# Performance work log

Hardware: AMD Instinct MI355X
Metric: run time of the kernel (lower is better)

The kernel has to match this reference:

```python
import jax, jax.numpy as jnp
import numpy as np

D_MODEL = 2048
NUM_HEADS = 16
HEAD_DIM = D_MODEL // NUM_HEADS  # 128
WINDOW = 1024
BATCH = 2
SEQ = 2048
NEG_INF = -1e9


def setup_inputs() -> dict:
    key = jax.random.key(0)
    ks = jax.random.split(key, 6)
    x = jax.random.normal(ks[0], (BATCH, SEQ, D_MODEL), dtype=jnp.float32)
    # RoPE frequencies (llama-style, theta=10000)
    inv_freq = 1.0 / (10000.0 ** (jnp.arange(0, HEAD_DIM, 2, dtype=jnp.float32) / HEAD_DIM))
    angles = jnp.arange(SEQ, dtype=jnp.float32)[:, None] * inv_freq[None, :]  # [S, hd/2]
    freqs_cos = jnp.cos(angles)
    freqs_sin = jnp.sin(angles)
    # additive causal mask [S, S]
    i = jnp.arange(SEQ)[:, None]
    j = jnp.arange(SEQ)[None, :]
    mask = jnp.where(j <= i, 0.0, NEG_INF).astype(jnp.float32)
    scale = 1.0 / np.sqrt(D_MODEL)
    w_q = jax.random.normal(ks[1], (D_MODEL, D_MODEL), dtype=jnp.float32) * scale
    w_k = jax.random.normal(ks[2], (D_MODEL, D_MODEL), dtype=jnp.float32) * scale
    w_v = jax.random.normal(ks[3], (D_MODEL, D_MODEL), dtype=jnp.float32) * scale
    w_o = jax.random.normal(ks[4], (D_MODEL, D_MODEL), dtype=jnp.float32) * scale
    return {"x": x, "freqs_cos": freqs_cos, "freqs_sin": freqs_sin, "mask": mask,
            "w_q": w_q, "w_k": w_k, "w_v": w_v, "w_o": w_o}


def _apply_rope(t, cos, sin):
    # t: [B, S, H, hd]; cos/sin: [S, hd/2]. Pairwise complex rotation.
    B, S, H, hd = t.shape
    tr = t.reshape(B, S, H, hd // 2, 2)
    a, b = tr[..., 0], tr[..., 1]
    c = cos[None, :, None, :]
    s = sin[None, :, None, :]
    out = jnp.stack([a * c - b * s, a * s + b * c], axis=-1)
    return out.reshape(B, S, H, hd)


def reference(x, freqs_cos, freqs_sin, mask, w_q, w_k, w_v, w_o):
    B, S, D = x.shape
    H, hd = NUM_HEADS, HEAD_DIM
    xq = (x @ w_q).reshape(B, S, H, hd)
    xk = (x @ w_k).reshape(B, S, H, hd)
    xv = (x @ w_v).reshape(B, S, H, hd)
    xq = _apply_rope(xq, freqs_cos, freqs_sin)
    xk = _apply_rope(xk, freqs_cos, freqs_sin)
    # scores: [B, H, S, S]
    scores = jnp.einsum("bqhd,bkhd->bhqk", xq, xk) / jnp.sqrt(jnp.asarray(hd, x.dtype))
    scores = scores + mask[None, None, :, :]
    # sliding-window mask: attend only to positions within WINDOW behind query
    i = jnp.arange(S)[:, None]
    j = jnp.arange(S)[None, :]
    sliding = (i - j >= 0) & (i - j < WINDOW)
    scores = jnp.where(sliding[None, None], scores, NEG_INF)
    probs = jax.nn.softmax(scores, axis=-1).astype(xq.dtype)
    out = jnp.einsum("bhqk,bkhd->bqhd", probs, xv).reshape(B, S, D)
    return out @ w_o
```

## Files before the change

kernel.cpp:

```cpp
#include <hip/hip_runtime.h>
#include <hip/hip_bf16.h>

typedef __attribute__((ext_vector_type(8))) short bf16x8;
typedef __attribute__((ext_vector_type(4))) float f32x4;
typedef unsigned short u16;
typedef unsigned int u32;

#define SEQ 2048
#define DMODEL 2048
#define NH 16
#define HD 128
#define NBATCH 2
#define WINDOW 1024

__device__ __forceinline__ float bf2f(u16 v) {
    union { u32 u; float f; } x; x.u = ((u32)v) << 16; return x.f;
}
__device__ __forceinline__ u16 f2bf(float f) {
    union { float f; u32 u; } x; x.f = f;
    u32 u = x.u;
    u32 r = (u + 0x7fffu + ((u >> 16) & 1u)) >> 16;
    return (u16)r;
}

__global__ __launch_bounds__(256) void cvt_f32_bf16(
    const float* __restrict__ in, u16* __restrict__ out)
{
    long i = ((long)blockIdx.x * 256 + threadIdx.x) * 8;
    float4 a = *(const float4*)(in + i);
    float4 b = *(const float4*)(in + i + 4);
    u16 v[8] = {f2bf(a.x), f2bf(a.y), f2bf(a.z), f2bf(a.w),
                f2bf(b.x), f2bf(b.y), f2bf(b.z), f2bf(b.w)};
    *(uint4*)(out + i) = *(uint4*)v;
}

__global__ __launch_bounds__(256) void transpose_f32_bf16(
    const float* __restrict__ in, u16* __restrict__ out, int R, int C)
{
    __shared__ u16 tile[64 * 72];
    const int c0 = blockIdx.x * 64, r0 = blockIdx.y * 64;
    const int t = threadIdx.x;
#pragma unroll
    for (int i = 0; i < 4; ++i) {
        int ch = i * 256 + t;
        int r = ch >> 4, c4 = (ch & 15) * 4;
        float4 v = *(const float4*)(in + (long)(r0 + r) * C + c0 + c4);
        tile[r * 72 + c4 + 0] = f2bf(v.x);
        tile[r * 72 + c4 + 1] = f2bf(v.y);
        tile[r * 72 + c4 + 2] = f2bf(v.z);
        tile[r * 72 + c4 + 3] = f2bf(v.w);
    }
    __syncthreads();
#pragma unroll
    for (int i = 0; i < 4; ++i) {
        int ch = i * 256 + t;
        int oc = ch >> 4, sg = (ch & 15) * 4;
        u16 vals[4];
#pragma unroll
        for (int j = 0; j < 4; ++j) vals[j] = tile[(sg + j) * 72 + oc];
        *(uint2*)(out + (long)(c0 + oc) * R + r0 + sg) = *(uint2*)vals;
    }
}

#define GLD16(gp, lp) __builtin_amdgcn_global_load_lds( \
    (const __attribute__((address_space(1))) u32*)(gp), \
    (__attribute__((address_space(3))) u32*)(lp), 16, 0, 0)
#define BAR() __builtin_amdgcn_s_barrier()
#define WAITV(n) asm volatile("s_waitcnt vmcnt(" #n ")" ::: "memory")

template <int MODE>
__global__ __launch_bounds__(512, 2) void gemm256(
    const u16* __restrict__ A, const u16* __restrict__ Bt,
    u16* __restrict__ OutB, float* __restrict__ OutF,
    const float* __restrict__ cosb, const float* __restrict__ sinb)
{
    extern __shared__ u16 sm[];
    const int t = threadIdx.x;
    const int w = t >> 6, l = t & 63;
    const int g = l >> 4, l15 = l & 15;
    const int wr = w >> 1, wc = w & 1;

    const int NWG = (MODE == 1) ? 768 : 256;
    const int cpx = NWG / 8;
    int bid = blockIdx.x;
    int wg = (bid & 7) * cpx + (bid >> 3);
    int z, m_t, n_t;
    if (MODE == 1) { z = wg >> 8; int rem = wg & 255; n_t = rem >> 4; m_t = rem & 15; }
    else           { z = 0; n_t = wg >> 4; m_t = wg & 15; }
    const int m0 = m_t * 256, n0 = n_t * 128;
    const u16* Ab = A + (long)m0 * 2048;
    const u16* Bb = Bt + (long)z * (2048L * 2048) + (long)n0 * 2048;

    const int r0 = t >> 3;
    const int kk16 = (t & 7) ^ (r0 & 7);
    const long g_off = (long)r0 * 2048 + kk16 * 8;
    const int lds_l = w * 512;
    const int sw = (l15 & 7) << 3;

#define STAGE(bufS_, ktS_) do { \
    const u16* _ga = Ab + (long)(ktS_) * 64 + g_off; \
    u16* _la = sm + (bufS_) * 24576 + lds_l; \
    GLD16(_ga,              _la); \
    GLD16(_ga +  64 * 2048, _la + 4096); \
    GLD16(_ga + 128 * 2048, _la + 8192); \
    GLD16(_ga + 192 * 2048, _la + 12288); \
    const u16* _gb = Bb + (long)(ktS_) * 64 + g_off; \
    u16* _lb = sm + (bufS_) * 24576 + 16384 + lds_l; \
    GLD16(_gb,              _lb); \
    GLD16(_gb + 64 * 2048,  _lb + 4096); \
} while (0)

    bf16x8 af[4][2], bfr[2][2];
    f32x4 acc[4][4] = {};

#define LDA_ALL(bufv) { const u16* _ba = sm + (bufv) * 24576; \
    _Pragma("unroll") for (int i = 0; i < 4; ++i) { \
        int row = wr * 64 + i * 16 + l15; \
        _Pragma("unroll") for (int kx = 0; kx < 2; ++kx) \
            af[i][kx] = *(const bf16x8*)(_ba + row * 64 + ((kx * 32 + g * 8) ^ sw)); } }

#define LDB_H(q, bufv) { const u16* _bb = sm + (bufv) * 24576 + 16384; \
    _Pragma("unroll") for (int j = 0; j < 2; ++j) { \
        int row = wc * 64 + (q) * 32 + j * 16 + l15; \
        _Pragma("unroll") for (int kx = 0; kx < 2; ++kx) \
            bfr[j][kx] = *(const bf16x8*)(_bb + row * 64 + ((kx * 32 + g * 8) ^ sw)); } }

#define MM(q) { __builtin_amdgcn_s_setprio(1); \
    _Pragma("unroll") for (int i = 0; i < 4; ++i) \
    _Pragma("unroll") for (int j = 0; j < 2; ++j) \
    _Pragma("unroll") for (int kx = 0; kx < 2; ++kx) \
        acc[i][(q) * 2 + j] = __builtin_amdgcn_mfma_f32_16x16x32_bf16( \
            af[i][kx], bfr[j][kx], acc[i][(q) * 2 + j], 0, 0, 0); \
    __builtin_amdgcn_s_setprio(0); }

    STAGE(0, 0); STAGE(1, 1);
    WAITV(6); BAR();

    int buf = 0, bufS = 2;
#pragma unroll 1
    for (int kt = 0; kt < 32; ++kt) {
        const int ktS = (kt + 2 <= 31) ? (kt + 2) : 31;
        LDA_ALL(buf); LDB_H(0, buf);
        STAGE(bufS, ktS);
        BAR(); MM(0); BAR();
        LDB_H(1, buf);
        WAITV(6);
        BAR(); MM(1); BAR();
        buf  = (buf  == 2) ? 0 : buf + 1;
        bufS = (bufS == 2) ? 0 : bufS + 1;
    }

#pragma unroll
    for (int mt = 0; mt < 4; ++mt) {
#pragma unroll
        for (int nt = 0; nt < 4; ++nt) {
#pragma unroll
            for (int r = 0; r < 4; ++r) {
                int m = m0 + wr * 64 + mt * 16 + g * 4 + r;
                int n = n0 + wc * 64 + nt * 16 + l15;
                float v = acc[mt][nt][r];
                if (MODE == 0) {
                    OutF[(long)m * 2048 + n] = v;
                } else {
                    int b = m >> 11, s = m & 2047;
                    int h = n >> 7,  d = n & 127;
                    float pv = __shfl_xor(v, 1);
                    if (z < 2) {
                        int p = d >> 1;
                        float cc = cosb[s * 64 + p];
                        float ss = sinb[s * 64 + p];
                        v = ((d & 1) == 0) ? (v * cc - pv * ss) : (pv * ss + v * cc);
                    }
                    long zoff = (long)z * (NBATCH * NH * SEQ * HD);
                    if (z == 2)
                        OutB[zoff + ((long)(b * NH + h) * HD + d) * SEQ + s] = f2bf(v);
                    else
                        OutB[zoff + ((long)(b * NH + h) * SEQ + s) * HD + d] = f2bf(v);
                }
            }
        }
    }
#undef STAGE
#undef LDA_ALL
#undef LDB_H
#undef MM
}

__global__ __launch_bounds__(256, 2) void attn_kernel(
    const u16* __restrict__ Q,
    const u16* __restrict__ K,
    const u16* __restrict__ Vt,
    u16* __restrict__ Out)
{
    __shared__ u16 k_lds[64 * 136];
    __shared__ u16 vt_lds[128 * 72];
    __shared__ u16 p_lds[4 * 16 * 72];
    const int t = threadIdx.x, w = t >> 6, l = t & 63;
    const int g = l >> 4, l15 = l & 15;
    const int q0 = blockIdx.x * 64;
    const int bh = blockIdx.y;
    const int qbase = q0 + w * 16;
    const u16* Qb = Q + (long)bh * SEQ * HD;
    const u16* Kb = K + (long)bh * SEQ * HD;
    const u16* Vb = Vt + (long)bh * HD * SEQ;
    u16* pw = p_lds + w * 16 * 72;

    bf16x8 qf[4];
#pragma unroll
    for (int kk = 0; kk < 4; ++kk)
        qf[kk] = *(const bf16x8*)(Qb + (long)(qbase + l15) * HD + kk * 32 + g * 8);

    f32x4 of[8] = {};
    float mrow[4] = {-1e30f, -1e30f, -1e30f, -1e30f};
    float lrow[4] = {0.f, 0.f, 0.f, 0.f};
    const float scale = 0.088388347648318447f;

    const int t0 = (q0 >= WINDOW) ? ((q0 - (WINDOW - 1)) >> 6) : 0;
    const int t1 = q0 >> 6;

    for (int kt = t0; kt <= t1; ++kt) {
        const int kv0 = kt * 64;
#pragma unroll
        for (int i = 0; i < 4; ++i) {
            int ch = i * 256 + t;
            { int r = ch >> 4, c = (ch & 15) * 8;
              *(uint4*)(k_lds + r * 136 + c) = *(const uint4*)(Kb + (long)(kv0 + r) * HD + c); }
            { int r = ch >> 3, c = (ch & 7) * 8;
              *(uint4*)(vt_lds + r * 72 + c) = *(const uint4*)(Vb + (long)r * SEQ + kv0 + c); }
        }
        __syncthreads();

        f32x4 sf[4] = {};
#pragma unroll
        for (int kk = 0; kk < 4; ++kk) {
#pragma unroll
            for (int nt = 0; nt < 4; ++nt) {
                bf16x8 kf = *(const bf16x8*)(k_lds + (nt * 16 + l15) * 136 + kk * 32 + g * 8);
                sf[nt] = __builtin_amdgcn_mfma_f32_16x16x32_bf16(qf[kk], kf, sf[nt], 0, 0, 0);
            }
        }
        const bool full = (kv0 + 63 <= qbase) && ((qbase + 15) - kv0 < WINDOW);
#pragma unroll
        for (int nt = 0; nt < 4; ++nt)
#pragma unroll
            for (int r = 0; r < 4; ++r) {
                float s = sf[nt][r] * scale;
                if (!full) {
                    int q = qbase + g * 4 + r;
                    int kv = kv0 + nt * 16 + l15;
                    bool ok = (kv <= q) && (q - kv < WINDOW);
                    s = ok ? s : -1e30f;
                }
                sf[nt][r] = s;
            }
        float fr[4];
#pragma unroll
        for (int r = 0; r < 4; ++r) {
            float v = fmaxf(fmaxf(sf[0][r], sf[1][r]), fmaxf(sf[2][r], sf[3][r]));
            v = fmaxf(v, __shfl_xor(v, 1));
            v = fmaxf(v, __shfl_xor(v, 2));
            v = fmaxf(v, __shfl_xor(v, 4));
            v = fmaxf(v, __shfl_xor(v, 8));
            float mn = fmaxf(mrow[r], v);
            fr[r] = __expf(mrow[r] - mn);
            mrow[r] = mn;
        }
        float rs[4] = {0.f, 0.f, 0.f, 0.f};
#pragma unroll
        for (int nt = 0; nt < 4; ++nt)
#pragma unroll
            for (int r = 0; r < 4; ++r) {
                float p = __expf(sf[nt][r] - mrow[r]);
                rs[r] += p;
                pw[(g * 4 + r) * 72 + nt * 16 + l15] = f2bf(p);
            }
#pragma unroll
        for (int r = 0; r < 4; ++r) {
            float v = rs[r];
            v += __shfl_xor(v, 1);
            v += __shfl_xor(v, 2);
            v += __shfl_xor(v, 4);
            v += __shfl_xor(v, 8);
            lrow[r] = lrow[r] * fr[r] + v;
        }
#pragma unroll
        for (int nd = 0; nd < 8; ++nd)
#pragma unroll
            for (int r = 0; r < 4; ++r) of[nd][r] *= fr[r];
#pragma unroll
        for (int kk = 0; kk < 2; ++kk) {
            bf16x8 pa = *(const bf16x8*)(pw + l15 * 72 + kk * 32 + g * 8);
#pragma unroll
            for (int nd = 0; nd < 8; ++nd) {
                bf16x8 vb = *(const bf16x8*)(vt_lds + (nd * 16 + l15) * 72 + kk * 32 + g * 8);
                of[nd] = __builtin_amdgcn_mfma_f32_16x16x32_bf16(pa, vb, of[nd], 0, 0, 0);
            }
        }
        __syncthreads();
    }
    const int b = bh >> 4, h = bh & 15;
#pragma unroll
    for (int r = 0; r < 4; ++r) {
        float inv = 1.0f / lrow[r];
        int q = qbase + g * 4 + r;
        u16* orow = Out + ((long)(b * SEQ + q)) * DMODEL + h * HD;
#pragma unroll
        for (int nd = 0; nd < 8; ++nd)
            orow[nd * 16 + l15] = f2bf(of[nd][r] * inv);
    }
}

extern "C" void kernel_launch(void* const* d_in, const int* in_sizes, int n_in,
                              void* d_out, int out_size, void* d_ws, size_t ws_size,
                              hipStream_t stream) {
    (void)in_sizes; (void)n_in; (void)out_size; (void)ws_size;
    const float* x    = (const float*)d_in[0];
    const float* fcos = (const float*)d_in[1];
    const float* fsin = (const float*)d_in[2];
    const float* wq = (const float*)d_in[4];
    const float* wk = (const float*)d_in[5];
    const float* wv = (const float*)d_in[6];
    const float* wo = (const float*)d_in[7];

    u16* ws = (u16*)d_ws;
    const long WT = 2048L * 2048;
    u16* xb  = ws;
    u16* wtq = xb + 8388608L;
    u16* wtk = wtq + WT;
    u16* wtv = wtk + WT;
    u16* wto = wtv + WT;
    u16* qkv = wto + WT;
    u16* q_ws = qkv;
    u16* k_ws = qkv + 8388608L;
    u16* vt_ws = qkv + 16777216L;
    u16* attn_ws = qkv + 25165824L;

    hipFuncSetAttribute(reinterpret_cast<const void*>(gemm256<1>),
                        hipFuncAttributeMaxDynamicSharedMemorySize, 147456);
    hipFuncSetAttribute(reinterpret_cast<const void*>(gemm256<0>),
                        hipFuncAttributeMaxDynamicSharedMemorySize, 147456);

    dim3 blk(256);
    cvt_f32_bf16<<<4096, blk, 0, stream>>>(x, xb);
    transpose_f32_bf16<<<dim3(32, 32), blk, 0, stream>>>(wq, wtq, 2048, 2048);
    transpose_f32_bf16<<<dim3(32, 32), blk, 0, stream>>>(wk, wtk, 2048, 2048);
    transpose_f32_bf16<<<dim3(32, 32), blk, 0, stream>>>(wv, wtv, 2048, 2048);
    transpose_f32_bf16<<<dim3(32, 32), blk, 0, stream>>>(wo, wto, 2048, 2048);
    gemm256<1><<<768, 512, 147456, stream>>>(xb, wtq, qkv, nullptr, fcos, fsin);
    attn_kernel<<<dim3(32, 32), blk, 0, stream>>>(q_ws, k_ws, vt_ws, attn_ws);
    gemm256<0><<<256, 512, 147456, stream>>>(attn_ws, wto, nullptr, (float*)d_out,
                                             nullptr, nullptr);
}
```

Baseline: 449.6 us.

## Software-pipeline GEMM main loop with split k-halves and a single barrier

Restructures the gemm256 k-loop so LDS fragment reads for the next k-half and the next tile are interleaved with MFMA blocks, using even/odd register sets and sched_barrier fences. Global-to-LDS staging is split into three pieces spread across the four MFMA groups, and the per-iteration barriers drop from four to one. The aim is to hide LDS read latency and barrier stalls behind matrix math. In exchange it needs more fragment registers and relies on careful wait counts to keep the triple-buffered LDS correct.

```diff
diff --git a/kernel.cpp b/kernel.cpp
--- a/kernel.cpp
+++ b/kernel.cpp
@@ -67,6 +67,8 @@
     (__attribute__((address_space(3))) u32*)(lp), 16, 0, 0)
 #define BAR() __builtin_amdgcn_s_barrier()
 #define WAITV(n) asm volatile("s_waitcnt vmcnt(" #n ")" ::: "memory")
+#define LGKM0() asm volatile("s_waitcnt lgkmcnt(0)" ::: "memory")
+#define SCHED0() __builtin_amdgcn_sched_barrier(0)
 
 template <int MODE>
 __global__ __launch_bounds__(512, 2) void gemm256(
@@ -97,58 +99,72 @@
     const int lds_l = w * 512;
     const int sw = (l15 & 7) << 3;
 
-#define STAGE(bufS_, ktS_) do { \
-    const u16* _ga = Ab + (long)(ktS_) * 64 + g_off; \
+#define STAGE_A01(bufS_, ktS_) { const u16* _ga = Ab + (long)(ktS_) * 64 + g_off; \
     u16* _la = sm + (bufS_) * 24576 + lds_l; \
-    GLD16(_ga,              _la); \
-    GLD16(_ga +  64 * 2048, _la + 4096); \
-    GLD16(_ga + 128 * 2048, _la + 8192); \
-    GLD16(_ga + 192 * 2048, _la + 12288); \
-    const u16* _gb = Bb + (long)(ktS_) * 64 + g_off; \
+    GLD16(_ga, _la); GLD16(_ga + 64 * 2048, _la + 4096); }
+#define STAGE_A23(bufS_, ktS_) { const u16* _ga = Ab + (long)(ktS_) * 64 + g_off; \
+    u16* _la = sm + (bufS_) * 24576 + lds_l; \
+    GLD16(_ga + 128 * 2048, _la + 8192); GLD16(_ga + 192 * 2048, _la + 12288); }
+#define STAGE_B01(bufS_, ktS_) { const u16* _gb = Bb + (long)(ktS_) * 64 + g_off; \
     u16* _lb = sm + (bufS_) * 24576 + 16384 + lds_l; \
-    GLD16(_gb,              _lb); \
-    GLD16(_gb + 64 * 2048,  _lb + 4096); \
-} while (0)
-
-    bf16x8 af[4][2], bfr[2][2];
+    GLD16(_gb, _lb); GLD16(_gb + 64 * 2048, _lb + 4096); }
+
+    bf16x8 af_e[4], af_o[4], b_e[2], b_o[2];
     f32x4 acc[4][4] = {};
 
-#define LDA_ALL(bufv) { const u16* _ba = sm + (bufv) * 24576; \
+#define RD_A(dst, kx, bufv) { const u16* _ba = sm + (bufv) * 24576; \
     _Pragma("unroll") for (int i = 0; i < 4; ++i) { \
         int row = wr * 64 + i * 16 + l15; \
-        _Pragma("unroll") for (int kx = 0; kx < 2; ++kx) \
-            af[i][kx] = *(const bf16x8*)(_ba + row * 64 + ((kx * 32 + g * 8) ^ sw)); } }
-
-#define LDB_H(q, bufv) { const u16* _bb = sm + (bufv) * 24576 + 16384; \
+        dst[i] = *(const bf16x8*)(_ba + row * 64 + (((kx) * 32 + g * 8) ^ sw)); } }
+
+#define RD_B(dst, kx, nh, bufv) { const u16* _bb = sm + (bufv) * 24576 + 16384; \
     _Pragma("unroll") for (int j = 0; j < 2; ++j) { \
-        int row = wc * 64 + (q) * 32 + j * 16 + l15; \
-        _Pragma("unroll") for (int kx = 0; kx < 2; ++kx) \
-            bfr[j][kx] = *(const bf16x8*)(_bb + row * 64 + ((kx * 32 + g * 8) ^ sw)); } }
-
-#define MM(q) { __builtin_amdgcn_s_setprio(1); \
+        int row = wc * 64 + (nh) * 32 + j * 16 + l15; \
+        dst[j] = *(const bf16x8*)(_bb + row * 64 + (((kx) * 32 + g * 8) ^ sw)); } }
+
+#define MM8(afv, bv, nh) { __builtin_amdgcn_s_setprio(1); \
     _Pragma("unroll") for (int i = 0; i < 4; ++i) \
     _Pragma("unroll") for (int j = 0; j < 2; ++j) \
-    _Pragma("unroll") for (int kx = 0; kx < 2; ++kx) \
-        acc[i][(q) * 2 + j] = __builtin_amdgcn_mfma_f32_16x16x32_bf16( \
-            af[i][kx], bfr[j][kx], acc[i][(q) * 2 + j], 0, 0, 0); \
+        acc[i][(nh) * 2 + j] = __builtin_amdgcn_mfma_f32_16x16x32_bf16( \
+            afv[i], bv[j], acc[i][(nh) * 2 + j], 0, 0, 0); \
     __builtin_amdgcn_s_setprio(0); }
 
-    STAGE(0, 0); STAGE(1, 1);
-    WAITV(6); BAR();
+    STAGE_A01(0, 0); STAGE_A23(0, 0); STAGE_B01(0, 0);
+    STAGE_A01(1, 1); STAGE_A23(1, 1); STAGE_B01(1, 1);
+    WAITV(6); SCHED0(); BAR();
+    RD_A(af_e, 0, 0); RD_B(b_e, 0, 0, 0);
 
     int buf = 0, bufS = 2;
 #pragma unroll 1
     for (int kt = 0; kt < 32; ++kt) {
         const int ktS = (kt + 2 <= 31) ? (kt + 2) : 31;
-        LDA_ALL(buf); LDB_H(0, buf);
-        STAGE(bufS, ktS);
-        BAR(); MM(0); BAR();
-        LDB_H(1, buf);
-        WAITV(6);
-        BAR(); MM(1); BAR();
-        buf  = (buf  == 2) ? 0 : buf + 1;
+        const int bufN = (buf == 2) ? 0 : buf + 1;
+        RD_A(af_o, 1, buf); RD_B(b_o, 1, 0, buf);
+        STAGE_A01(bufS, ktS);
+        SCHED0();
+        MM8(af_e, b_e, 0);
+        SCHED0();
+        RD_B(b_e, 0, 1, buf);
+        STAGE_A23(bufS, ktS);
+        SCHED0();
+        MM8(af_o, b_o, 0);
+        SCHED0();
+        RD_B(b_o, 1, 1, buf);
+        STAGE_B01(bufS, ktS);
+        SCHED0();
+        MM8(af_e, b_e, 1);
+        SCHED0();
+        LGKM0(); SCHED0();
+        WAITV(6); SCHED0();
+        BAR();
+        if (kt < 31) { RD_A(af_e, 0, bufN); RD_B(b_e, 0, 0, bufN); }
+        SCHED0();
+        MM8(af_o, b_o, 1);
+        SCHED0();
+        buf = bufN;
         bufS = (bufS == 2) ? 0 : bufS + 1;
     }
+    WAITV(0);
 
 #pragma unroll
     for (int mt = 0; mt < 4; ++mt) {
@@ -180,10 +196,12 @@
             }
         }
     }
-#undef STAGE
-#undef LDA_ALL
-#undef LDB_H
-#undef MM
+#undef STAGE_A01
+#undef STAGE_A23
+#undef STAGE_B01
+#undef RD_A
+#undef RD_B
+#undef MM8
 }
 
 __global__ __launch_bounds__(256, 2) void attn_kernel(
```

Result: faster. 439.2 us (-2.3%).
